# Kernel tuning notes

Hardware: AMD Instinct MI355X
Metric: run time of the kernel (lower is better)

Reference implementation:

```python
import jax, jax.numpy as jnp
import numpy as np

B, L_Q, L_K = 16, 256, 256
Q_DIM, K_DIM, H_DIM, V_DIM = 256, 256, 128, 128


def setup_inputs() -> dict:
    key = jax.random.key(0)
    k1, k2, k3, k4, k5, k6 = jax.random.split(key, 6)
    query = jax.random.normal(k1, (B, L_Q, Q_DIM), dtype=jnp.float32)
    key_t = jax.random.normal(k2, (B, L_K, K_DIM), dtype=jnp.float32)
    value = jax.random.normal(k3, (B, L_Q, V_DIM), dtype=jnp.float32)
    # Linear weights stored as [in, out] for x @ W (equivalent to torch Linear, no bias)
    Wq = jax.random.normal(k4, (Q_DIM, H_DIM), dtype=jnp.float32) / np.sqrt(Q_DIM)
    Wk = jax.random.normal(k5, (K_DIM, H_DIM), dtype=jnp.float32) / np.sqrt(K_DIM)
    v = jax.random.uniform(k6, (H_DIM,), dtype=jnp.float32, minval=-0.1, maxval=0.1)
    return {"query": query, "key": key_t, "value": value, "Wq": Wq, "Wk": Wk, "v": v}


def reference(query, key, value, Wq, Wk, v):
    # Project first (equivalent to applying Linear after the expand, but cheaper):
    qp = jnp.einsum("bqd,dh->bqh", query, Wq)  # [B, l_q, h]
    kp = jnp.einsum("bkd,dh->bkh", key, Wk)    # [B, l_k, h]
    # score[b, k, q] = tanh(qp[b,q] + kp[b,k]) . v  -> [B, l_k, l_q]
    score = jnp.einsum("bkqh,h->bkq", jnp.tanh(qp[:, None, :, :] + kp[:, :, None, :]), v)
    attention = jax.nn.softmax(score, axis=-1)  # softmax over query positions (dim -1)
    context = jnp.einsum("bkq,bqv->bkv", attention, value)  # bmm
    return context, attention
```

## Files before the change

### kernel.cpp

```cpp
#include <hip/hip_runtime.h>

#define B_  16
#define LQ  256
#define LK  256
#define QD  256
#define HD  128
#define VD  128

#define SCALE2 2.8853900817779268f
#define L2E    1.4426950408889634f
#define CTX_SIZE (B_ * LK * VD)

__device__ __forceinline__ float fast_exp2(float x) { return __builtin_amdgcn_exp2f(x); }
__device__ __forceinline__ float fast_rcp(float x)  { return __builtin_amdgcn_rcpf(x); }

__global__ __launch_bounds__(256, 4) void proj_kernel(const float* __restrict__ query,
                                                      const float* __restrict__ key,
                                                      const float* __restrict__ Wq,
                                                      const float* __restrict__ Wk,
                                                      float4* __restrict__ qe4,
                                                      float4* __restrict__ ke4)
{
    __shared__ float  Xs[8][258];
    __shared__ float4 part[4][32][9];

    const int t = threadIdx.x;
    const bool isQ = (blockIdx.x < 512);
    const int blk  = isQ ? blockIdx.x : (blockIdx.x - 512);
    const int rows0 = blk * 8;
    const float* X = isQ ? query : key;
    const float4* W4 = (const float4*)(isQ ? Wq : Wk);

    {
        const int r = t >> 5;
        const int c = (t & 31) * 8;
        const float4 x0 = *(const float4*)(X + (size_t)(rows0 + r) * QD + c);
        const float4 x1 = *(const float4*)(X + (size_t)(rows0 + r) * QD + c + 4);
        *(float4*)&Xs[r][c]     = x0;
        *(float4*)&Xs[r][c + 4] = x1;
    }
    __syncthreads();

    const int w    = t >> 6;
    const int lane = t & 63;
    const int hg   = lane & 31;
    const int mb   = lane >> 5;

    float4 acc[4];
#pragma unroll
    for (int i = 0; i < 4; i++) acc[i] = make_float4(0.f, 0.f, 0.f, 0.f);

    const int kbase = w * 64;
#pragma unroll 4
    for (int kk = 0; kk < 64; kk += 2) {
        const int k = kbase + kk;
        const float4 w0 = W4[(size_t)k * 32 + hg];
        const float4 w1 = W4[(size_t)(k + 1) * 32 + hg];
#pragma unroll
        for (int mi = 0; mi < 4; mi++) {
            const float2 x = *(const float2*)&Xs[mb + 2 * mi][k];
            acc[mi].x += x.x * w0.x + x.y * w1.x;
            acc[mi].y += x.x * w0.y + x.y * w1.y;
            acc[mi].z += x.x * w0.z + x.y * w1.z;
            acc[mi].w += x.x * w0.w + x.y * w1.w;
        }
    }
#pragma unroll
    for (int mi = 0; mi < 4; mi++) part[w][hg][mb + 2 * mi] = acc[mi];
    __syncthreads();

    if (isQ) {
        const int q8 = t & 7, h4 = t >> 3;
        float4 s = part[0][h4][q8];
        const float4 p1 = part[1][h4][q8];
        const float4 p2 = part[2][h4][q8];
        const float4 p3 = part[3][h4][q8];
        s.x += p1.x + p2.x + p3.x;  s.y += p1.y + p2.y + p3.y;
        s.z += p1.z + p2.z + p3.z;  s.w += p1.w + p2.w + p3.w;
        const float4 e = make_float4(fast_exp2(s.x * SCALE2), fast_exp2(s.y * SCALE2),
                                     fast_exp2(s.z * SCALE2), fast_exp2(s.w * SCALE2));
        const int row = rows0 + q8, b = row >> 8, q = row & 255;
        qe4[((size_t)b * 32 + h4) * 256 + q] = e;
    } else {
        const int h4 = t & 31, m = t >> 5;
        float4 s = part[0][h4][m];
        const float4 p1 = part[1][h4][m];
        const float4 p2 = part[2][h4][m];
        const float4 p3 = part[3][h4][m];
        s.x += p1.x + p2.x + p3.x;  s.y += p1.y + p2.y + p3.y;
        s.z += p1.z + p2.z + p3.z;  s.w += p1.w + p2.w + p3.w;
        const float4 e = make_float4(fast_exp2(s.x * SCALE2), fast_exp2(s.y * SCALE2),
                                     fast_exp2(s.z * SCALE2), fast_exp2(s.w * SCALE2));
        ke4[(size_t)(rows0 + m) * 32 + h4] = e;
    }
}

__global__ __launch_bounds__(256, 4) void attn_kernel(const float4* __restrict__ qe4,
                                                      const float4* __restrict__ ke4,
                                                      const float* __restrict__ v,
                                                      const float* __restrict__ value,
                                                      float* __restrict__ out)
{
    __shared__ float  score_s[4][260];
    __shared__ float  attn_T[256][4];
    __shared__ float2 partc[4][4][64];

    const int t  = threadIdx.x;
    const int b  = blockIdx.x >> 6;
    const int k0 = (blockIdx.x & 63) << 2;

    const float4* qb = qe4 + (size_t)b * 32 * 256;
    const float4* kb = ke4 + ((size_t)b * LK + k0) * 32;
    const float4* v4 = (const float4*)v;

    float acc0 = 0.f, acc1 = 0.f, acc2 = 0.f, acc3 = 0.f;
    const int q = t;
#pragma unroll 4
    for (int h4 = 0; h4 < 32; h4++) {
        const float4 qv = qb[(size_t)h4 * 256 + q];
        const float4 vv = v4[h4];
        const float4 ka = kb[0 * 32 + h4];
        const float4 kc = kb[1 * 32 + h4];
        const float4 kd = kb[2 * 32 + h4];
        const float4 kf = kb[3 * 32 + h4];
        acc0 += vv.x * fast_rcp(qv.x * ka.x + 1.f) + vv.y * fast_rcp(qv.y * ka.y + 1.f)
              + vv.z * fast_rcp(qv.z * ka.z + 1.f) + vv.w * fast_rcp(qv.w * ka.w + 1.f);
        acc1 += vv.x * fast_rcp(qv.x * kc.x + 1.f) + vv.y * fast_rcp(qv.y * kc.y + 1.f)
              + vv.z * fast_rcp(qv.z * kc.z + 1.f) + vv.w * fast_rcp(qv.w * kc.w + 1.f);
        acc2 += vv.x * fast_rcp(qv.x * kd.x + 1.f) + vv.y * fast_rcp(qv.y * kd.y + 1.f)
              + vv.z * fast_rcp(qv.z * kd.z + 1.f) + vv.w * fast_rcp(qv.w * kd.w + 1.f);
        acc3 += vv.x * fast_rcp(qv.x * kf.x + 1.f) + vv.y * fast_rcp(qv.y * kf.y + 1.f)
              + vv.z * fast_rcp(qv.z * kf.z + 1.f) + vv.w * fast_rcp(qv.w * kf.w + 1.f);
    }
    float sumv = 0.f;
#pragma unroll
    for (int h4 = 0; h4 < 32; h4++) {
        const float4 vv = v4[h4];
        sumv += vv.x + vv.y + vv.z + vv.w;
    }

    score_s[0][q] = sumv - 2.f * acc0;
    score_s[1][q] = sumv - 2.f * acc1;
    score_s[2][q] = sumv - 2.f * acc2;
    score_s[3][q] = sumv - 2.f * acc3;
    __syncthreads();

    const int w = t >> 6, lane = t & 63;
    {
        float x0 = score_s[w][lane];
        float x1 = score_s[w][lane + 64];
        float x2 = score_s[w][lane + 128];
        float x3 = score_s[w][lane + 192];
        float m = fmaxf(fmaxf(x0, x1), fmaxf(x2, x3));
#pragma unroll
        for (int off = 32; off >= 1; off >>= 1) m = fmaxf(m, __shfl_xor(m, off));
        float e0 = fast_exp2((x0 - m) * L2E);
        float e1 = fast_exp2((x1 - m) * L2E);
        float e2 = fast_exp2((x2 - m) * L2E);
        float e3 = fast_exp2((x3 - m) * L2E);
        float s = e0 + e1 + e2 + e3;
#pragma unroll
        for (int off = 32; off >= 1; off >>= 1) s += __shfl_xor(s, off);
        const float rs = fast_rcp(s);
        e0 *= rs; e1 *= rs; e2 *= rs; e3 *= rs;
        attn_T[lane][w]       = e0;
        attn_T[lane + 64][w]  = e1;
        attn_T[lane + 128][w] = e2;
        attn_T[lane + 192][w] = e3;
        float* ao = out + CTX_SIZE + ((size_t)(b * LK + k0 + w)) * LQ;
        ao[lane]       = e0;
        ao[lane + 64]  = e1;
        ao[lane + 128] = e2;
        ao[lane + 192] = e3;
    }
    __syncthreads();

    {
        const int vd2 = lane * 2;
        const float* valb = value + (size_t)b * LQ * VD;
        float2 c0 = {0.f, 0.f}, c1 = {0.f, 0.f}, c2 = {0.f, 0.f}, c3 = {0.f, 0.f};
#pragma unroll 4
        for (int i = 0; i < 64; i++) {
            const int q2 = (w << 6) + i;
            const float4 a = *(const float4*)&attn_T[q2][0];
            const float2 vv = *(const float2*)(valb + (size_t)q2 * VD + vd2);
            c0.x += a.x * vv.x; c0.y += a.x * vv.y;
            c1.x += a.y * vv.x; c1.y += a.y * vv.y;
            c2.x += a.z * vv.x; c2.y += a.z * vv.y;
            c3.x += a.w * vv.x; c3.y += a.w * vv.y;
        }
        partc[w][0][lane] = c0;
        partc[w][1][lane] = c1;
        partc[w][2][lane] = c2;
        partc[w][3][lane] = c3;
    }
    __syncthreads();
    {
        const int kg = t >> 6, l2 = t & 63;
        const float2 p0 = partc[0][kg][l2];
        const float2 p1 = partc[1][kg][l2];
        const float2 p2 = partc[2][kg][l2];
        const float2 p3 = partc[3][kg][l2];
        float2 s;
        s.x = p0.x + p1.x + p2.x + p3.x;
        s.y = p0.y + p1.y + p2.y + p3.y;
        *(float2*)(out + ((size_t)(b * LK + k0 + kg)) * VD + l2 * 2) = s;
    }
}

extern "C" void kernel_launch(void* const* d_in, const int* in_sizes, int n_in,
                              void* d_out, int out_size, void* d_ws, size_t ws_size,
                              hipStream_t stream)
{
    const float* query = (const float*)d_in[0];
    const float* key   = (const float*)d_in[1];
    const float* value = (const float*)d_in[2];
    const float* Wq    = (const float*)d_in[3];
    const float* Wk    = (const float*)d_in[4];
    const float* v     = (const float*)d_in[5];
    float* out = (float*)d_out;

    float4* qe4 = (float4*)d_ws;
    float4* ke4 = qe4 + (size_t)B_ * 32 * 256;

    proj_kernel<<<dim3(1024), 256, 0, stream>>>(query, key, Wq, Wk, qe4, ke4);
    attn_kernel<<<dim3(1024), 256, 0, stream>>>(qe4, ke4, v, value, out);
}
```

Baseline: 109.1 us.

## Use 1024-thread blocks handling 8 keys with 2 keys per thread

Measured after the change: 138.0 us. +26.5%, slower.

```diff
diff --git a/kernel.cpp b/kernel.cpp
--- a/kernel.cpp
+++ b/kernel.cpp
@@ -95,42 +95,38 @@
     }
 }
 
-__global__ __launch_bounds__(256, 4) void attn_kernel(const float4* __restrict__ qe4,
-                                                      const float4* __restrict__ ke4,
-                                                      const float* __restrict__ v,
-                                                      const float* __restrict__ value,
-                                                      float* __restrict__ out)
+__global__ __launch_bounds__(1024, 8) void attn_kernel(const float4* __restrict__ qe4,
+                                                       const float4* __restrict__ ke4,
+                                                       const float* __restrict__ v,
+                                                       const float* __restrict__ value,
+                                                       float* __restrict__ out)
 {
-    __shared__ float  score_s[4][260];
-    __shared__ float  attn_T[256][4];
-    __shared__ float2 partc[4][4][64];
+    __shared__ float  score_s[8][260];
+    __shared__ float  attn_T[256][9];
+    __shared__ float2 partc[2][8][64];
 
     const int t  = threadIdx.x;
-    const int b  = blockIdx.x >> 6;
-    const int k0 = (blockIdx.x & 63) << 2;
+    const int b  = blockIdx.x >> 5;
+    const int k0 = (blockIdx.x & 31) << 3;
+
+    const int kq = t >> 8;
+    const int q  = t & 255;
 
     const float4* qb = qe4 + (size_t)b * 32 * 256;
-    const float4* kb = ke4 + ((size_t)b * LK + k0) * 32;
+    const float4* kb = ke4 + ((size_t)b * LK + k0 + kq * 2) * 32;
     const float4* v4 = (const float4*)v;
 
-    float acc0 = 0.f, acc1 = 0.f, acc2 = 0.f, acc3 = 0.f;
-    const int q = t;
+    float acc0 = 0.f, acc1 = 0.f;
 #pragma unroll 4
     for (int h4 = 0; h4 < 32; h4++) {
         const float4 qv = qb[(size_t)h4 * 256 + q];
         const float4 vv = v4[h4];
-        const float4 ka = kb[0 * 32 + h4];
-        const float4 kc = kb[1 * 32 + h4];
-        const float4 kd = kb[2 * 32 + h4];
-        const float4 kf = kb[3 * 32 + h4];
+        const float4 ka = kb[h4];
+        const float4 kc = kb[32 + h4];
         acc0 += vv.x * fast_rcp(qv.x * ka.x + 1.f) + vv.y * fast_rcp(qv.y * ka.y + 1.f)
               + vv.z * fast_rcp(qv.z * ka.z + 1.f) + vv.w * fast_rcp(qv.w * ka.w + 1.f);
         acc1 += vv.x * fast_rcp(qv.x * kc.x + 1.f) + vv.y * fast_rcp(qv.y * kc.y + 1.f)
               + vv.z * fast_rcp(qv.z * kc.z + 1.f) + vv.w * fast_rcp(qv.w * kc.w + 1.f);
-        acc2 += vv.x * fast_rcp(qv.x * kd.x + 1.f) + vv.y * fast_rcp(qv.y * kd.y + 1.f)
-              + vv.z * fast_rcp(qv.z * kd.z + 1.f) + vv.w * fast_rcp(qv.w * kd.w + 1.f);
-        acc3 += vv.x * fast_rcp(qv.x * kf.x + 1.f) + vv.y * fast_rcp(qv.y * kf.y + 1.f)
-              + vv.z * fast_rcp(qv.z * kf.z + 1.f) + vv.w * fast_rcp(qv.w * kf.w + 1.f);
     }
     float sumv = 0.f;
 #pragma unroll
@@ -138,15 +134,12 @@
         const float4 vv = v4[h4];
         sumv += vv.x + vv.y + vv.z + vv.w;
     }
-
-    score_s[0][q] = sumv - 2.f * acc0;
-    score_s[1][q] = sumv - 2.f * acc1;
-    score_s[2][q] = sumv - 2.f * acc2;
-    score_s[3][q] = sumv - 2.f * acc3;
-    __syncthreads();
-
-    const int w = t >> 6, lane = t & 63;
-    {
+    score_s[kq * 2 + 0][q] = sumv - 2.f * acc0;
+    score_s[kq * 2 + 1][q] = sumv - 2.f * acc1;
+    __syncthreads();
+
+    if (t < 512) {
+        const int w = t >> 6, lane = t & 63;
         float x0 = score_s[w][lane];
         float x1 = score_s[w][lane + 64];
         float x2 = score_s[w][lane + 128];
@@ -176,35 +169,31 @@
     __syncthreads();
 
     {
+        const int w = t >> 6, lane = t & 63;
+        const int k = w & 7, qh = w >> 3;
         const int vd2 = lane * 2;
         const float* valb = value + (size_t)b * LQ * VD;
-        float2 c0 = {0.f, 0.f}, c1 = {0.f, 0.f}, c2 = {0.f, 0.f}, c3 = {0.f, 0.f};
+        float2 c = {0.f, 0.f};
+        const int qbase = qh * 128;
 #pragma unroll 4
-        for (int i = 0; i < 64; i++) {
-            const int q2 = (w << 6) + i;
-            const float4 a = *(const float4*)&attn_T[q2][0];
+        for (int i = 0; i < 128; i++) {
+            const int q2 = qbase + i;
+            const float a = attn_T[q2][k];
             const float2 vv = *(const float2*)(valb + (size_t)q2 * VD + vd2);
-            c0.x += a.x * vv.x; c0.y += a.x * vv.y;
-            c1.x += a.y * vv.x; c1.y += a.y * vv.y;
-            c2.x += a.z * vv.x; c2.y += a.z * vv.y;
-            c3.x += a.w * vv.x; c3.y += a.w * vv.y;
+            c.x += a * vv.x;
+            c.y += a * vv.y;
         }
-        partc[w][0][lane] = c0;
-        partc[w][1][lane] = c1;
-        partc[w][2][lane] = c2;
-        partc[w][3][lane] = c3;
-    }
-    __syncthreads();
-    {
-        const int kg = t >> 6, l2 = t & 63;
-        const float2 p0 = partc[0][kg][l2];
-        const float2 p1 = partc[1][kg][l2];
-        const float2 p2 = partc[2][kg][l2];
-        const float2 p3 = partc[3][kg][l2];
+        partc[qh][k][lane] = c;
+    }
+    __syncthreads();
+    if (t < 512) {
+        const int k = t >> 6, l = t & 63;
+        const float2 p0 = partc[0][k][l];
+        const float2 p1 = partc[1][k][l];
         float2 s;
-        s.x = p0.x + p1.x + p2.x + p3.x;
-        s.y = p0.y + p1.y + p2.y + p3.y;
-        *(float2*)(out + ((size_t)(b * LK + k0 + kg)) * VD + l2 * 2) = s;
+        s.x = p0.x + p1.x;
+        s.y = p0.y + p1.y;
+        *(float2*)(out + ((size_t)(b * LK + k0 + k)) * VD + l * 2) = s;
     }
 }
 
@@ -224,5 +213,5 @@
     float4* ke4 = qe4 + (size_t)B_ * 32 * 256;
 
     proj_kernel<<<dim3(1024), 256, 0, stream>>>(query, key, Wq, Wk, qe4, ke4);
-    attn_kernel<<<dim3(1024), 256, 0, stream>>>(qe4, ke4, v, value, out);
+    attn_kernel<<<dim3(512), 1024, 0, stream>>>(qe4, ke4, v, value, out);
 }
```
